# Kernel tuning notes

Hardware: AMD Instinct MI355X
Metric: run time of the kernel (lower is better)

Reference implementation:

```python
import jax, jax.numpy as jnp
import numpy as np

B, N, C, HEADS = 8, 1024, 768, 12
HW = 32  # H = W = 32, so H*W == N


def _layernorm(x, g, b, eps=1e-5):
    mu = x.mean(-1, keepdims=True)
    var = ((x - mu) ** 2).mean(-1, keepdims=True)
    return (x - mu) * jax.lax.rsqrt(var + eps) * g + b


def setup_inputs() -> dict:
    key = jax.random.key(0)
    ks = jax.random.split(key, 6)
    w = lambda k, shape: jax.random.normal(k, shape, dtype=jnp.float32) * 0.02
    return {
        "x": jax.random.normal(ks[0], (B, N, C), dtype=jnp.float32),
        "y": jax.random.normal(ks[1], (B, C, HW, HW), dtype=jnp.float32),
        "q_w": w(ks[2], (C, C)),
        "q_b": jnp.zeros((C,), jnp.float32),
        "kv_w": w(ks[3], (2 * C, C)),
        "kv_b": jnp.zeros((2 * C,), jnp.float32),
        "proj_w": w(ks[4], (C, C)),
        "proj_b": jnp.zeros((C,), jnp.float32),
        "ln_g": jnp.ones((C,), jnp.float32),
        "ln_b": jnp.zeros((C,), jnp.float32),
        "H": HW,
        "W": HW,
    }


def reference(x, y, q_w, q_b, kv_w, kv_b, proj_w, proj_b, ln_g, ln_b, H, W):
    Bn, Nn, Cn = x.shape
    hd = Cn // HEADS
    scale = hd ** -0.5  # qk_scale=None, c_ratio=1 -> head_dim**-0.5

    # gating tensors from y
    y1 = y.reshape(Bn, Cn, H * W).transpose(0, 2, 1)          # [B, N, C]
    y2 = _layernorm(y1, ln_g, ln_b)
    yq = jax.nn.sigmoid(y2 @ q_w.T + q_b)                      # [B, N, C]
    ykv = jax.nn.sigmoid(y2 @ kv_w.T + kv_b)                   # [B, N, 2C]

    # gated q: q2 = q0 + q0*yq
    q0 = x @ q_w.T + q_b
    q = (q0 + q0 * yq).reshape(Bn, Nn, HEADS, hd).transpose(0, 2, 1, 3)  # [B,h,N,d]

    # gated kv: kv2 = kv0*ykv + ykv
    kv0 = x @ kv_w.T + kv_b
    kv = (kv0 * ykv + ykv).reshape(Bn, Nn, 2, HEADS, hd).transpose(2, 0, 3, 1, 4)
    k, v = kv[0], kv[1]                                        # [B,h,N,d] each

    attn = jax.nn.softmax(jnp.einsum("bhqd,bhkd->bhqk", q, k) * scale, axis=-1)
    out = jnp.einsum("bhqk,bhkd->bhqd", attn, v)
    out = out.transpose(0, 2, 1, 3).reshape(Bn, Nn, Cn)
    return out @ proj_w.T + proj_b
```

## Files before the change

kernel.cpp:

```cpp
#include <hip/hip_runtime.h>
#include <stdint.h>

typedef __attribute__((ext_vector_type(4))) float f4;
typedef __attribute__((ext_vector_type(8))) short bf16x8;
typedef __attribute__((ext_vector_type(4))) unsigned short u16x4;
typedef unsigned short u16;

#define B_ 8
#define N_ 1024
#define C_ 768
#define NH 12
#define HD 64

__device__ __forceinline__ float bf2f(u16 v) {
  union { unsigned u; float f; } x; x.u = ((unsigned)v) << 16; return x.f;
}
__device__ __forceinline__ u16 f2bf(float f) {
  union { float f; unsigned u; } x; x.f = f;
  unsigned r = x.u + 0x7FFFu + ((x.u >> 16) & 1u);
  return (u16)(r >> 16);
}
__device__ __forceinline__ void g2l16(const u16* g, const u16* l) {
  __builtin_amdgcn_global_load_lds(
      (const __attribute__((address_space(1))) void*)(uintptr_t)g,
      (__attribute__((address_space(3))) void*)(uint32_t)(uintptr_t)l,
      16, 0, 0);
}

#define SW12() asm volatile("s_waitcnt vmcnt(12)" ::: "memory")
#define SW6()  asm volatile("s_waitcnt vmcnt(6)" ::: "memory")
#define SW4()  asm volatile("s_waitcnt vmcnt(4)" ::: "memory")
#define SW3()  asm volatile("s_waitcnt vmcnt(3)" ::: "memory")
#define SW0()  asm volatile("s_waitcnt vmcnt(0)" ::: "memory")
#define BARF()                              \
  do {                                      \
    __builtin_amdgcn_s_barrier();           \
    asm volatile("" ::: "memory");          \
    __builtin_amdgcn_sched_barrier(0);      \
  } while (0)

__global__ __launch_bounds__(256) void cvt_bf16(const float* __restrict__ s,
                                                u16* __restrict__ d, int n4) {
  int i = blockIdx.x * 256 + threadIdx.x;
  int stride = gridDim.x * 256;
  for (; i < n4; i += stride) {
    float4 v = ((const float4*)s)[i];
    u16x4 o;
    o.x = f2bf(v.x); o.y = f2bf(v.y); o.z = f2bf(v.z); o.w = f2bf(v.w);
    ((u16x4*)d)[i] = o;
  }
}

__global__ __launch_bounds__(256) void ln_stats(const float* __restrict__ y,
                                                float* __restrict__ mu,
                                                float* __restrict__ rs,
                                                int b0) {
  __shared__ float s1[4][64], s2[4][64];
  int t = threadIdx.x;
  int nl = t & 63, ch = t >> 6;
  int idx0 = b0 * N_ + blockIdx.x * 64;
  int b = idx0 >> 10, nb_ = idx0 & 1023;
  const float* p = y + (size_t)b * C_ * N_ + nb_ + nl;
  float s = 0.f, q = 0.f;
  int c0 = ch * 192;
  for (int c = c0; c < c0 + 192; ++c) {
    float v = p[(size_t)c * N_];
    s += v; q += v * v;
  }
  s1[ch][nl] = s; s2[ch][nl] = q;
  __syncthreads();
  if (t < 64) {
    float ts = s1[0][t] + s1[1][t] + s1[2][t] + s1[3][t];
    float tq = s2[0][t] + s2[1][t] + s2[2][t] + s2[3][t];
    float m = ts * (1.f / C_);
    float var = tq * (1.f / C_) - m * m;
    mu[idx0 + t] = m;
    rs[idx0 + t] = rsqrtf(fmaxf(var, 0.f) + 1e-5f);
  }
}

__global__ __launch_bounds__(256) void ln_apply(const float* __restrict__ y,
                                                const float* __restrict__ mu,
                                                const float* __restrict__ rs,
                                                const float* __restrict__ lg,
                                                const float* __restrict__ lb,
                                                u16* __restrict__ y2c,
                                                int b0) {
  __shared__ float tile[64][65];
  int t = threadIdx.x;
  int n0 = blockIdx.x * 64, c0 = blockIdx.y * 64;
  int bl = blockIdx.z, b = b0 + bl;
  int jc = (t & 15) * 4, ir = t >> 4;
  for (int r = 0; r < 4; ++r) {
    int i = ir + r * 16;
    float4 v = *(const float4*)(y + ((size_t)b * C_ + c0 + i) * N_ + n0 + jc);
    tile[i][jc] = v.x; tile[i][jc + 1] = v.y; tile[i][jc + 2] = v.z; tile[i][jc + 3] = v.w;
  }
  __syncthreads();
  for (int r = 0; r < 4; ++r) {
    int i = ir + r * 16;
    int n = n0 + i;
    float m = mu[b * N_ + n], rr = rs[b * N_ + n];
    float g0 = lg[c0 + jc],     b0f = lb[c0 + jc];
    float g1 = lg[c0 + jc + 1], b1f = lb[c0 + jc + 1];
    float g2 = lg[c0 + jc + 2], b2f = lb[c0 + jc + 2];
    float g3 = lg[c0 + jc + 3], b3f = lb[c0 + jc + 3];
    u16x4 o;
    o.x = f2bf((tile[jc][i] - m) * rr * g0 + b0f);
    o.y = f2bf((tile[jc + 1][i] - m) * rr * g1 + b1f);
    o.z = f2bf((tile[jc + 2][i] - m) * rr * g2 + b2f);
    o.w = f2bf((tile[jc + 3][i] - m) * rr * g3 + b3f);
    *(u16x4*)(y2c + ((size_t)bl * N_ + n) * C_ + c0 + jc) = o;
  }
}

__global__ __launch_bounds__(256, 2) void gemm_gate(
    const u16* __restrict__ xbc, const u16* __restrict__ y2c,
    const u16* __restrict__ qwb, const u16* __restrict__ kvwb,
    const float* __restrict__ qb_, const float* __restrict__ kvb_,
    u16* __restrict__ o_q, u16* __restrict__ o_k, u16* __restrict__ o_vT) {
  __shared__ u16 smem[36864];
  int t = threadIdx.x, l = t & 63;
  int quad = l >> 4, l15 = l & 15;
  int w = t >> 6, wm = w & 1, wn = w >> 1;
  int m0l = blockIdx.x * 128;
  int n0l = blockIdx.y * 128;

  const u16* wp; const float* bp; int sel, h0;
  if (n0l < C_) {
    wp = qwb + (size_t)n0l * C_; bp = qb_ + n0l; sel = 0; h0 = n0l >> 6;
  } else {
    int nk = n0l - C_;
    wp = kvwb + (size_t)nk * C_; bp = kvb_ + nk;
    sel = (nk < C_) ? 1 : 2;
    h0 = ((sel == 2) ? nk - C_ : nk) >> 6;
  }

  f4 accx[4][4], accy[4][4];
  for (int i = 0; i < 4; ++i)
    for (int j = 0; j < 4; ++j) {
      accx[i][j] = (f4){0.f, 0.f, 0.f, 0.f};
      accy[i][j] = (f4){0.f, 0.f, 0.f, 0.f};
    }

  int row = t >> 2;
  int colS = (((t & 3) ^ (row & 3)) * 8);
  const u16* gx = xbc + (size_t)(m0l + row) * C_ + colS;
  const u16* gy = y2c + (size_t)(m0l + row) * C_ + colS;
  const u16* gw = wp + (size_t)row * C_ + colS;
  int rsl = (quad ^ (l15 & 3)) * 8;

#define STAGE_G(OFF, kk)                                   \
  do {                                                     \
    u16* p_ = smem + (OFF);                                \
    g2l16(gx + (kk),           p_ + t * 8);                \
    g2l16(gx + (kk) + 64 * C_, p_ + 2048 + t * 8);         \
    g2l16(gy + (kk),           p_ + 4096 + t * 8);         \
    g2l16(gy + (kk) + 64 * C_, p_ + 6144 + t * 8);         \
    g2l16(gw + (kk),           p_ + 8192 + t * 8);         \
    g2l16(gw + (kk) + 64 * C_, p_ + 10240 + t * 8);        \
  } while (0)

#define COMPUTE_G(OFF)                                                        \
  do {                                                                        \
    const u16* base = smem + (OFF);                                           \
    bf16x8 afx[4], afy[4], bfr[4];                                            \
    for (int i = 0; i < 4; ++i) {                                             \
      int ra = (wm * 64 + i * 16 + l15) * 32 + rsl;                           \
      afx[i] = *(const bf16x8*)&base[ra];                                     \
      afy[i] = *(const bf16x8*)&base[4096 + ra];                              \
      int rb = (wn * 64 + i * 16 + l15) * 32 + rsl;                           \
      bfr[i] = *(const bf16x8*)&base[8192 + rb];                              \
    }                                                                         \
    for (int i = 0; i < 4; ++i)                                               \
      for (int j = 0; j < 4; ++j) {                                           \
        accx[i][j] = __builtin_amdgcn_mfma_f32_16x16x32_bf16(afx[i], bfr[j], accx[i][j], 0, 0, 0); \
        accy[i][j] = __builtin_amdgcn_mfma_f32_16x16x32_bf16(afy[i], bfr[j], accy[i][j], 0, 0, 0); \
      }                                                                       \
  } while (0)

#define STEP_G(i, OFF)                                        \
  do {                                                        \
    COMPUTE_G(OFF);                                           \
    BARF();                                                   \
    if ((i) < 21)      { STAGE_G(OFF, ((i) + 3) * 32); SW12(); } \
    else if ((i) == 21) SW6();                                \
    else if ((i) == 22) SW0();                                \
    BARF();                                                   \
  } while (0)

  STAGE_G(0, 0);
  STAGE_G(12288, 32);
  STAGE_G(24576, 64);
  SW12();
  BARF();
#pragma unroll
  for (int n = 0; n < 24; n += 3) {
    STEP_G(n, 0);
    STEP_G(n + 1, 12288);
    STEP_G(n + 2, 24576);
  }
#undef STEP_G
#undef STAGE_G
#undef COMPUTE_G

  const int PITCH = 136;
  for (int j = 0; j < 4; ++j) {
    int cloc = wn * 64 + j * 16 + l15;
    float bias = bp[cloc];
    for (int i = 0; i < 4; ++i) {
      int rb0 = wm * 64 + i * 16 + quad * 4;
      for (int r = 0; r < 4; ++r) {
        int rloc = rb0 + r;
        float vx = accx[i][j][r] + bias;
        float vy = accy[i][j][r] + bias;
        float gg = 1.f / (1.f + __expf(-vy));
        float val = (sel == 0) ? vx * (1.f + gg) : gg * (vx + 1.f);
        u16 bv = f2bf(val);
        if (sel == 2) smem[cloc * PITCH + rloc] = bv;
        else          smem[rloc * PITCH + cloc] = bv;
      }
    }
  }
  __syncthreads();
  {
    int rr = t >> 1, hh = t & 1;
    const u16* src = smem + rr * PITCH + hh * 64;
    u16* dst;
    if (sel == 2) {
      int h = h0 + (rr >> 6), d = rr & 63;
      int bl = m0l >> 10, nbase = m0l & 1023;
      dst = o_vT + (size_t)((bl * NH + h) * HD + d) * N_ + nbase + hh * 64;
    } else {
      int gml = m0l + rr;
      int bl = gml >> 10, n = gml & 1023;
      int h = h0 + hh;
      dst = (sel == 0 ? o_q : o_k) + (size_t)((bl * NH + h) * N_ + n) * HD;
    }
    for (int c = 0; c < 8; ++c) {
      bf16x8 v = *(const bf16x8*)(src + c * 8);
      *(bf16x8*)(dst + c * 8) = v;
    }
  }
}

__global__ __launch_bounds__(256) void attn(const u16* __restrict__ qoc,
                                            const u16* __restrict__ koc,
                                            const u16* __restrict__ vTc,
                                            u16* __restrict__ aoc) {
  __shared__ u16 Qs[4096], Ks[8192], Vs[8192];
  __shared__ u16 Ps[64 * 72];
  int t = threadIdx.x, l = t & 63, w = t >> 6;
  int quad = l >> 4, l15 = l & 15;
  int bhl = blockIdx.y;
  int bl = bhl / NH, h = bhl % NH;
  int q0 = blockIdx.x * 64;
  int sr = t >> 3;
  int swo = ((t & 7) ^ (sr & 7)) * 8;
  const u16* qbp = qoc + ((size_t)bhl * N_ + q0) * HD;
  const u16* kb = koc + (size_t)bhl * N_ * HD;
  const u16* vb = vTc + (size_t)bhl * HD * N_;

#define STAGE_KV(OFF, key0)                                                   \
  do {                                                                        \
    g2l16(kb + (size_t)((key0) + sr) * HD + swo,      Ks + (OFF) + t * 8);    \
    g2l16(kb + (size_t)((key0) + 32 + sr) * HD + swo, Ks + (OFF) + 2048 + t * 8); \
    g2l16(vb + (size_t)sr * N_ + (key0) + swo,        Vs + (OFF) + t * 8);    \
    g2l16(vb + (size_t)(32 + sr) * N_ + (key0) + swo, Vs + (OFF) + 2048 + t * 8); \
  } while (0)

  g2l16(qbp + sr * HD + swo,        Qs + t * 8);
  g2l16(qbp + (32 + sr) * HD + swo, Qs + 2048 + t * 8);
  STAGE_KV(0, 0);
  STAGE_KV(4096, 64);
  SW4();
  BARF();

  int sA = (quad ^ (l15 & 7)) * 8;
  int sB = sA ^ 32;
  bf16x8 aq0 = *(const bf16x8*)&Qs[(w * 16 + l15) * 64 + sA];
  bf16x8 aq1 = *(const bf16x8*)&Qs[(w * 16 + l15) * 64 + sB];
  f4 o[4];
  for (int i = 0; i < 4; ++i) o[i] = (f4){0.f, 0.f, 0.f, 0.f};
  f4 ls = (f4){0.f, 0.f, 0.f, 0.f};
  bf16x8 ones;
  for (int i = 0; i < 8; ++i) ones[i] = (short)0x3F80;

#define TILE_STEP(KOFF)                                                       \
  do {                                                                        \
    f4 s_[4];                                                                 \
    __builtin_amdgcn_s_setprio(1);                                            \
    for (int ni = 0; ni < 4; ++ni) {                                          \
      bf16x8 b0v = *(const bf16x8*)&Ks[(KOFF) + (ni * 16 + l15) * 64 + sA];   \
      bf16x8 b1v = *(const bf16x8*)&Ks[(KOFF) + (ni * 16 + l15) * 64 + sB];   \
      f4 z = (f4){0.f, 0.f, 0.f, 0.f};                                        \
      z = __builtin_amdgcn_mfma_f32_16x16x32_bf16(aq0, b0v, z, 0, 0, 0);      \
      z = __builtin_amdgcn_mfma_f32_16x16x32_bf16(aq1, b1v, z, 0, 0, 0);      \
      s_[ni] = z;                                                             \
    }                                                                         \
    __builtin_amdgcn_s_setprio(0);                                            \
    for (int ni = 0; ni < 4; ++ni)                                            \
      for (int r = 0; r < 4; ++r)                                             \
        Ps[(w * 16 + quad * 4 + r) * 72 + ni * 16 + l15] =                    \
            f2bf(__expf(s_[ni][r] * 0.125f));                                 \
    bf16x8 ap0 = *(const bf16x8*)&Ps[(w * 16 + l15) * 72 + quad * 8];         \
    bf16x8 ap1 = *(const bf16x8*)&Ps[(w * 16 + l15) * 72 + 32 + quad * 8];    \
    __builtin_amdgcn_s_setprio(1);                                            \
    for (int ni = 0; ni < 4; ++ni) {                                          \
      bf16x8 b0v = *(const bf16x8*)&Vs[(KOFF) + (ni * 16 + l15) * 64 + sA];   \
      bf16x8 b1v = *(const bf16x8*)&Vs[(KOFF) + (ni * 16 + l15) * 64 + sB];   \
      o[ni] = __builtin_amdgcn_mfma_f32_16x16x32_bf16(ap0, b0v, o[ni], 0, 0, 0); \
      o[ni] = __builtin_amdgcn_mfma_f32_16x16x32_bf16(ap1, b1v, o[ni], 0, 0, 0); \
    }                                                                         \
    ls = __builtin_amdgcn_mfma_f32_16x16x32_bf16(ap0, ones, ls, 0, 0, 0);     \
    ls = __builtin_amdgcn_mfma_f32_16x16x32_bf16(ap1, ones, ls, 0, 0, 0);     \
    __builtin_amdgcn_s_setprio(0);                                            \
  } while (0)

#pragma unroll
  for (int kt = 0; kt < 16; kt += 2) {
    TILE_STEP(0);
    BARF();
    if (kt + 2 < 16) { STAGE_KV(0, (kt + 2) * 64); SW4(); } else { SW0(); }
    BARF();
    TILE_STEP(4096);
    BARF();
    if (kt + 3 < 16) { STAGE_KV(4096, (kt + 3) * 64); SW4(); } else { SW0(); }
    BARF();
  }
#undef TILE_STEP
#undef STAGE_KV

  for (int ni = 0; ni < 4; ++ni)
    for (int r = 0; r < 4; ++r)
      Ps[(w * 16 + quad * 4 + r) * 72 + ni * 16 + l15] =
          f2bf(o[ni][r] / ls[r]);
  __syncthreads();
  {
    int rr = t >> 2, cc = t & 3;
    int n = q0 + rr;
    const u16* src = Ps + rr * 72 + cc * 16;
    u16* dst = aoc + ((size_t)bl * N_ + n) * C_ + h * HD + cc * 16;
    *(bf16x8*)dst = *(const bf16x8*)src;
    *(bf16x8*)(dst + 8) = *(const bf16x8*)(src + 8);
  }
}

__global__ __launch_bounds__(256, 2) void gemm_proj(const u16* __restrict__ aoc,
                                                    const u16* __restrict__ pwb,
                                                    const float* __restrict__ bias,
                                                    float* __restrict__ out,
                                                    int b0) {
  __shared__ u16 smem[18432];
  int t = threadIdx.x, l = t & 63;
  int quad = l >> 4, l15 = l & 15;
  int w = t >> 6, wm = w & 1, wn = w >> 1;
  int m0l = blockIdx.x * 128, n0 = blockIdx.y * 64;
  f4 acc[4][2];
  for (int i = 0; i < 4; ++i)
    for (int j = 0; j < 2; ++j) acc[i][j] = (f4){0.f, 0.f, 0.f, 0.f};
  int row = t >> 2;
  int colS = (((t & 3) ^ (row & 3)) * 8);
  const u16* ga = aoc + (size_t)(m0l + row) * C_ + colS;
  const u16* gw = pwb + (size_t)(n0 + row) * C_ + colS;
  int rsl = (quad ^ (l15 & 3)) * 8;

#define STAGE_P(OFF, kk)                                   \
  do {                                                     \
    u16* p_ = smem + (OFF);                                \
    g2l16(ga + (kk),           p_ + t * 8);                \
    g2l16(ga + (kk) + 64 * C_, p_ + 2048 + t * 8);         \
    g2l16(gw + (kk),           p_ + 4096 + t * 8);         \
  } while (0)

#define COMPUTE_P(OFF)                                                        \
  do {                                                                        \
    const u16* base = smem + (OFF);                                           \
    bf16x8 af[4], bfr[2];                                                     \
    for (int i = 0; i < 4; ++i)                                               \
      af[i] = *(const bf16x8*)&base[(wm * 64 + i * 16 + l15) * 32 + rsl];     \
    for (int j = 0; j < 2; ++j)                                               \
      bfr[j] = *(const bf16x8*)&base[4096 + (wn * 32 + j * 16 + l15) * 32 + rsl]; \
    for (int i = 0; i < 4; ++i)                                               \
      for (int j = 0; j < 2; ++j)                                             \
        acc[i][j] = __builtin_amdgcn_mfma_f32_16x16x32_bf16(af[i], bfr[j], acc[i][j], 0, 0, 0); \
  } while (0)

#define STEP_P(i, OFF)                                        \
  do {                                                        \
    COMPUTE_P(OFF);                                           \
    BARF();                                                   \
    if ((i) < 21)      { STAGE_P(OFF, ((i) + 3) * 32); SW6(); } \
    else if ((i) == 21) SW3();                                \
    else if ((i) == 22) SW0();                                \
    BARF();                                                   \
  } while (0)

  STAGE_P(0, 0);
  STAGE_P(6144, 32);
  STAGE_P(12288, 64);
  SW6();
  BARF();
#pragma unroll
  for (int n = 0; n < 24; n += 3) {
    STEP_P(n, 0);
    STEP_P(n + 1, 6144);
    STEP_P(n + 2, 12288);
  }
#undef STEP_P
#undef STAGE_P
#undef COMPUTE_P

  for (int j = 0; j < 2; ++j) {
    int gcol = n0 + wn * 32 + j * 16 + l15;
    float bv = bias[gcol];
    for (int i = 0; i < 4; ++i) {
      int rbase = m0l + wm * 64 + i * 16 + quad * 4;
      for (int r = 0; r < 4; ++r)
        __builtin_nontemporal_store(acc[i][j][r] + bv,
                                    &out[(size_t)(b0 * N_ + rbase + r) * C_ + gcol]);
    }
  }
}

extern "C" void kernel_launch(void* const* d_in, const int* in_sizes, int n_in,
                              void* d_out, int out_size, void* d_ws, size_t ws_size,
                              hipStream_t stream) {
  const float* x   = (const float*)d_in[0];
  const float* y   = (const float*)d_in[1];
  const float* qw  = (const float*)d_in[2];
  const float* qb  = (const float*)d_in[3];
  const float* kvw = (const float*)d_in[4];
  const float* kvb = (const float*)d_in[5];
  const float* pw  = (const float*)d_in[6];
  const float* pb  = (const float*)d_in[7];
  const float* lg  = (const float*)d_in[8];
  const float* lb  = (const float*)d_in[9];

  char* ws = (char*)d_ws;
  float* mu = (float*)(ws);
  float* rs = (float*)(ws + 32768);
  u16* qwb  = (u16*)(ws + 65536);
  u16* kvwb = (u16*)(ws + 1245184);
  u16* pwb  = (u16*)(ws + 3604480);
  const size_t BASE2 = 4784128;
  const size_t PER_B = 1572864;

  int nb = 1;
  for (int c = 8; c >= 1; c >>= 1) {
    if (BASE2 + 5 * (size_t)c * PER_B <= ws_size) { nb = c; break; }
  }
  u16* xbc = (u16*)(ws + BASE2);
  u16* y2c = (u16*)(ws + BASE2 + (size_t)nb * PER_B);
  u16* qoc = (u16*)(ws + BASE2 + 2 * (size_t)nb * PER_B);
  u16* koc = (u16*)(ws + BASE2 + 3 * (size_t)nb * PER_B);
  u16* vTc = (u16*)(ws + BASE2 + 4 * (size_t)nb * PER_B);
  u16* aoc = xbc;

  cvt_bf16<<<dim3(576), dim3(256), 0, stream>>>(qw, qwb, 147456);
  cvt_bf16<<<dim3(1152), dim3(256), 0, stream>>>(kvw, kvwb, 294912);
  cvt_bf16<<<dim3(576), dim3(256), 0, stream>>>(pw, pwb, 147456);

  for (int b0 = 0; b0 < B_; b0 += nb) {
    cvt_bf16<<<dim3(768 * nb), dim3(256), 0, stream>>>(
        x + (size_t)b0 * N_ * C_, xbc, nb * 196608);
    ln_stats<<<dim3(16 * nb), dim3(256), 0, stream>>>(y, mu, rs, b0);
    ln_apply<<<dim3(16, 12, nb), dim3(256), 0, stream>>>(y, mu, rs, lg, lb, y2c, b0);
    gemm_gate<<<dim3(8 * nb, 18), dim3(256), 0, stream>>>(xbc, y2c, qwb, kvwb,
                                                          qb, kvb, qoc, koc, vTc);
    attn<<<dim3(16, 12 * nb), dim3(256), 0, stream>>>(qoc, koc, vTc, aoc);
    gemm_proj<<<dim3(8 * nb, 12), dim3(256), 0, stream>>>(aoc, pwb, pb, (float*)d_out, b0);
  }
}
```

Before: 285.3 us.

## Issue next-stage global loads before compute with one barrier per K step

The gated-projection and output-projection GEMM loops now issue the async global-to-LDS stage for step i+2 into the free third buffer before computing on the current buffer, then wait once and barrier once per step instead of twice. This keeps prefetch distance at two and cuts one barrier per iteration while loads overlap the MFMA work. The pragma unroll directives on these loops and the attention loop are also removed, which may change code size and scheduling. The risk is reduced in-flight prefetch depth, and loops that are no longer fully unrolled may lose compile-time evaluation of the (i) conditions.

```diff
diff --git a/kernel.cpp b/kernel.cpp
--- a/kernel.cpp
+++ b/kernel.cpp
@@ -27,7 +27,6 @@
       16, 0, 0);
 }
 
-#define SW12() asm volatile("s_waitcnt vmcnt(12)" ::: "memory")
 #define SW6()  asm volatile("s_waitcnt vmcnt(6)" ::: "memory")
 #define SW4()  asm volatile("s_waitcnt vmcnt(4)" ::: "memory")
 #define SW3()  asm volatile("s_waitcnt vmcnt(3)" ::: "memory")
@@ -179,26 +178,23 @@
       }                                                                       \
   } while (0)
 
-#define STEP_G(i, OFF)                                        \
+#define STEP_G(i, OFFC, OFFS)                                 \
   do {                                                        \
-    COMPUTE_G(OFF);                                           \
-    BARF();                                                   \
-    if ((i) < 21)      { STAGE_G(OFF, ((i) + 3) * 32); SW12(); } \
-    else if ((i) == 21) SW6();                                \
+    if ((i) <= 21) STAGE_G(OFFS, ((i) + 2) * 32);             \
+    COMPUTE_G(OFFC);                                          \
+    if ((i) <= 21)      SW6();                                \
     else if ((i) == 22) SW0();                                \
     BARF();                                                   \
   } while (0)
 
   STAGE_G(0, 0);
   STAGE_G(12288, 32);
-  STAGE_G(24576, 64);
-  SW12();
+  SW6();
   BARF();
-#pragma unroll
   for (int n = 0; n < 24; n += 3) {
-    STEP_G(n, 0);
-    STEP_G(n + 1, 12288);
-    STEP_G(n + 2, 24576);
+    STEP_G(n,     0,     24576);
+    STEP_G(n + 1, 12288, 0);
+    STEP_G(n + 2, 24576, 12288);
   }
 #undef STEP_G
 #undef STAGE_G
@@ -317,7 +313,6 @@
     __builtin_amdgcn_s_setprio(0);                                            \
   } while (0)
 
-#pragma unroll
   for (int kt = 0; kt < 16; kt += 2) {
     TILE_STEP(0);
     BARF();
@@ -386,26 +381,23 @@
         acc[i][j] = __builtin_amdgcn_mfma_f32_16x16x32_bf16(af[i], bfr[j], acc[i][j], 0, 0, 0); \
   } while (0)
 
-#define STEP_P(i, OFF)                                        \
+#define STEP_P(i, OFFC, OFFS)                                 \
   do {                                                        \
-    COMPUTE_P(OFF);                                           \
-    BARF();                                                   \
-    if ((i) < 21)      { STAGE_P(OFF, ((i) + 3) * 32); SW6(); } \
-    else if ((i) == 21) SW3();                                \
+    if ((i) <= 21) STAGE_P(OFFS, ((i) + 2) * 32);             \
+    COMPUTE_P(OFFC);                                          \
+    if ((i) <= 21)      SW3();                                \
     else if ((i) == 22) SW0();                                \
     BARF();                                                   \
   } while (0)
 
   STAGE_P(0, 0);
   STAGE_P(6144, 32);
-  STAGE_P(12288, 64);
-  SW6();
+  SW3();
   BARF();
-#pragma unroll
   for (int n = 0; n < 24; n += 3) {
-    STEP_P(n, 0);
-    STEP_P(n + 1, 6144);
-    STEP_P(n + 2, 12288);
+    STEP_P(n,     0,     12288);
+    STEP_P(n + 1, 6144,  0);
+    STEP_P(n + 2, 12288, 6144);
   }
 #undef STEP_P
 #undef STAGE_P
```

Result: no change. 285.5 us (+0.1%).

## Double attention query tile to 128 rows and simplify proj GEMM pipeline

Applied to the files above, without the earlier changes.

The attention kernel now handles 128 query rows per block: each wave keeps two 16-row query fragments and reuses every staged K/V tile for both, so K/V global loads per query are halved. The grid shrinks to 8 blocks per head, which lowers parallelism and raises register and LDS use. The projection GEMM also drops from triple to double buffering and removes its LDS XOR swizzle, which may bring back bank conflicts in exchange for less shared memory.

```diff
diff --git a/kernel.cpp b/kernel.cpp
--- a/kernel.cpp
+++ b/kernel.cpp
@@ -248,13 +248,13 @@
                                             const u16* __restrict__ koc,
                                             const u16* __restrict__ vTc,
                                             u16* __restrict__ aoc) {
-  __shared__ u16 Qs[4096], Ks[8192], Vs[8192];
-  __shared__ u16 Ps[64 * 72];
+  __shared__ u16 Qs[8192], Ks[8192], Vs[8192];
+  __shared__ u16 Ps[128 * 72];
   int t = threadIdx.x, l = t & 63, w = t >> 6;
   int quad = l >> 4, l15 = l & 15;
   int bhl = blockIdx.y;
   int bl = bhl / NH, h = bhl % NH;
-  int q0 = blockIdx.x * 64;
+  int q0 = blockIdx.x * 128;
   int sr = t >> 3;
   int swo = ((t & 7) ^ (sr & 7)) * 8;
   const u16* qbp = qoc + ((size_t)bhl * N_ + q0) * HD;
@@ -269,8 +269,10 @@
     g2l16(vb + (size_t)(32 + sr) * N_ + (key0) + swo, Vs + (OFF) + 2048 + t * 8); \
   } while (0)
 
-  g2l16(qbp + sr * HD + swo,        Qs + t * 8);
-  g2l16(qbp + (32 + sr) * HD + swo, Qs + 2048 + t * 8);
+  g2l16(qbp + (size_t)(sr) * HD + swo,       Qs + t * 8);
+  g2l16(qbp + (size_t)(32 + sr) * HD + swo,  Qs + 2048 + t * 8);
+  g2l16(qbp + (size_t)(64 + sr) * HD + swo,  Qs + 4096 + t * 8);
+  g2l16(qbp + (size_t)(96 + sr) * HD + swo,  Qs + 6144 + t * 8);
   STAGE_KV(0, 0);
   STAGE_KV(4096, 64);
   SW4();
@@ -278,46 +280,68 @@
 
   int sA = (quad ^ (l15 & 7)) * 8;
   int sB = sA ^ 32;
-  bf16x8 aq0 = *(const bf16x8*)&Qs[(w * 16 + l15) * 64 + sA];
-  bf16x8 aq1 = *(const bf16x8*)&Qs[(w * 16 + l15) * 64 + sB];
-  f4 o[4];
-  for (int i = 0; i < 4; ++i) o[i] = (f4){0.f, 0.f, 0.f, 0.f};
-  f4 ls = (f4){0.f, 0.f, 0.f, 0.f};
+  bf16x8 aq00 = *(const bf16x8*)&Qs[(w * 16 + l15) * 64 + sA];
+  bf16x8 aq01 = *(const bf16x8*)&Qs[(w * 16 + l15) * 64 + sB];
+  bf16x8 aq10 = *(const bf16x8*)&Qs[(64 + w * 16 + l15) * 64 + sA];
+  bf16x8 aq11 = *(const bf16x8*)&Qs[(64 + w * 16 + l15) * 64 + sB];
+  f4 o0[4], o1[4];
+  for (int i = 0; i < 4; ++i) {
+    o0[i] = (f4){0.f, 0.f, 0.f, 0.f};
+    o1[i] = (f4){0.f, 0.f, 0.f, 0.f};
+  }
+  f4 ls0 = (f4){0.f, 0.f, 0.f, 0.f};
+  f4 ls1 = (f4){0.f, 0.f, 0.f, 0.f};
   bf16x8 ones;
   for (int i = 0; i < 8; ++i) ones[i] = (short)0x3F80;
 
 #define TILE_STEP(KOFF)                                                       \
   do {                                                                        \
-    f4 s_[4];                                                                 \
+    f4 s0_[4], s1_[4];                                                        \
     __builtin_amdgcn_s_setprio(1);                                            \
+    _Pragma("unroll")                                                         \
     for (int ni = 0; ni < 4; ++ni) {                                          \
       bf16x8 b0v = *(const bf16x8*)&Ks[(KOFF) + (ni * 16 + l15) * 64 + sA];   \
       bf16x8 b1v = *(const bf16x8*)&Ks[(KOFF) + (ni * 16 + l15) * 64 + sB];   \
-      f4 z = (f4){0.f, 0.f, 0.f, 0.f};                                        \
-      z = __builtin_amdgcn_mfma_f32_16x16x32_bf16(aq0, b0v, z, 0, 0, 0);      \
-      z = __builtin_amdgcn_mfma_f32_16x16x32_bf16(aq1, b1v, z, 0, 0, 0);      \
-      s_[ni] = z;                                                             \
+      f4 z0 = (f4){0.f, 0.f, 0.f, 0.f};                                       \
+      z0 = __builtin_amdgcn_mfma_f32_16x16x32_bf16(aq00, b0v, z0, 0, 0, 0);   \
+      z0 = __builtin_amdgcn_mfma_f32_16x16x32_bf16(aq01, b1v, z0, 0, 0, 0);   \
+      s0_[ni] = z0;                                                           \
+      f4 z1 = (f4){0.f, 0.f, 0.f, 0.f};                                       \
+      z1 = __builtin_amdgcn_mfma_f32_16x16x32_bf16(aq10, b0v, z1, 0, 0, 0);   \
+      z1 = __builtin_amdgcn_mfma_f32_16x16x32_bf16(aq11, b1v, z1, 0, 0, 0);   \
+      s1_[ni] = z1;                                                           \
     }                                                                         \
     __builtin_amdgcn_s_setprio(0);                                            \
+    _Pragma("unroll")                                                         \
     for (int ni = 0; ni < 4; ++ni)                                            \
-      for (int r = 0; r < 4; ++r)                                             \
+      _Pragma("unroll")                                                       \
+      for (int r = 0; r < 4; ++r) {                                           \
         Ps[(w * 16 + quad * 4 + r) * 72 + ni * 16 + l15] =                    \
-            f2bf(__expf(s_[ni][r] * 0.125f));                                 \
-    bf16x8 ap0 = *(const bf16x8*)&Ps[(w * 16 + l15) * 72 + quad * 8];         \
-    bf16x8 ap1 = *(const bf16x8*)&Ps[(w * 16 + l15) * 72 + 32 + quad * 8];    \
+            f2bf(__expf(s0_[ni][r] * 0.125f));                                \
+        Ps[(64 + w * 16 + quad * 4 + r) * 72 + ni * 16 + l15] =               \
+            f2bf(__expf(s1_[ni][r] * 0.125f));                                \
+      }                                                                       \
+    bf16x8 ap00 = *(const bf16x8*)&Ps[(w * 16 + l15) * 72 + quad * 8];        \
+    bf16x8 ap01 = *(const bf16x8*)&Ps[(w * 16 + l15) * 72 + 32 + quad * 8];   \
+    bf16x8 ap10 = *(const bf16x8*)&Ps[(64 + w * 16 + l15) * 72 + quad * 8];   \
+    bf16x8 ap11 = *(const bf16x8*)&Ps[(64 + w * 16 + l15) * 72 + 32 + quad * 8]; \
     __builtin_amdgcn_s_setprio(1);                                            \
+    _Pragma("unroll")                                                         \
     for (int ni = 0; ni < 4; ++ni) {                                          \
       bf16x8 b0v = *(const bf16x8*)&Vs[(KOFF) + (ni * 16 + l15) * 64 + sA];   \
       bf16x8 b1v = *(const bf16x8*)&Vs[(KOFF) + (ni * 16 + l15) * 64 + sB];   \
-      o[ni] = __builtin_amdgcn_mfma_f32_16x16x32_bf16(ap0, b0v, o[ni], 0, 0, 0); \
-      o[ni] = __builtin_amdgcn_mfma_f32_16x16x32_bf16(ap1, b1v, o[ni], 0, 0, 0); \
+      o0[ni] = __builtin_amdgcn_mfma_f32_16x16x32_bf16(ap00, b0v, o0[ni], 0, 0, 0); \
+      o0[ni] = __builtin_amdgcn_mfma_f32_16x16x32_bf16(ap01, b1v, o0[ni], 0, 0, 0); \
+      o1[ni] = __builtin_amdgcn_mfma_f32_16x16x32_bf16(ap10, b0v, o1[ni], 0, 0, 0); \
+      o1[ni] = __builtin_amdgcn_mfma_f32_16x16x32_bf16(ap11, b1v, o1[ni], 0, 0, 0); \
     }                                                                         \
-    ls = __builtin_amdgcn_mfma_f32_16x16x32_bf16(ap0, ones, ls, 0, 0, 0);     \
-    ls = __builtin_amdgcn_mfma_f32_16x16x32_bf16(ap1, ones, ls, 0, 0, 0);     \
+    ls0 = __builtin_amdgcn_mfma_f32_16x16x32_bf16(ap00, ones, ls0, 0, 0, 0);  \
+    ls0 = __builtin_amdgcn_mfma_f32_16x16x32_bf16(ap01, ones, ls0, 0, 0, 0);  \
+    ls1 = __builtin_amdgcn_mfma_f32_16x16x32_bf16(ap10, ones, ls1, 0, 0, 0);  \
+    ls1 = __builtin_amdgcn_mfma_f32_16x16x32_bf16(ap11, ones, ls1, 0, 0, 0);  \
     __builtin_amdgcn_s_setprio(0);                                            \
   } while (0)
 
-#pragma unroll
   for (int kt = 0; kt < 16; kt += 2) {
     TILE_STEP(0);
     BARF();
@@ -332,17 +356,20 @@
 #undef STAGE_KV
 
   for (int ni = 0; ni < 4; ++ni)
-    for (int r = 0; r < 4; ++r)
+    for (int r = 0; r < 4; ++r) {
       Ps[(w * 16 + quad * 4 + r) * 72 + ni * 16 + l15] =
-          f2bf(o[ni][r] / ls[r]);
+          f2bf(o0[ni][r] / ls0[r]);
+      Ps[(64 + w * 16 + quad * 4 + r) * 72 + ni * 16 + l15] =
+          f2bf(o1[ni][r] / ls1[r]);
+    }
   __syncthreads();
   {
-    int rr = t >> 2, cc = t & 3;
+    int rr = t >> 1, cc = t & 1;
     int n = q0 + rr;
-    const u16* src = Ps + rr * 72 + cc * 16;
-    u16* dst = aoc + ((size_t)bl * N_ + n) * C_ + h * HD + cc * 16;
-    *(bf16x8*)dst = *(const bf16x8*)src;
-    *(bf16x8*)(dst + 8) = *(const bf16x8*)(src + 8);
+    const u16* src = Ps + rr * 72 + cc * 32;
+    u16* dst = aoc + ((size_t)bl * N_ + n) * C_ + h * HD + cc * 32;
+    for (int c = 0; c < 4; ++c)
+      *(bf16x8*)(dst + c * 8) = *(const bf16x8*)(src + c * 8);
   }
 }
 
@@ -351,7 +378,7 @@
                                                     const float* __restrict__ bias,
                                                     float* __restrict__ out,
                                                     int b0) {
-  __shared__ u16 smem[18432];
+  __shared__ u16 smem[12288];
   int t = threadIdx.x, l = t & 63;
   int quad = l >> 4, l15 = l & 15;
   int w = t >> 6, wm = w & 1, wn = w >> 1;
@@ -359,11 +386,9 @@
   f4 acc[4][2];
   for (int i = 0; i < 4; ++i)
     for (int j = 0; j < 2; ++j) acc[i][j] = (f4){0.f, 0.f, 0.f, 0.f};
-  int row = t >> 2;
-  int colS = (((t & 3) ^ (row & 3)) * 8);
-  const u16* ga = aoc + (size_t)(m0l + row) * C_ + colS;
-  const u16* gw = pwb + (size_t)(n0 + row) * C_ + colS;
-  int rsl = (quad ^ (l15 & 3)) * 8;
+  int row = t >> 2, colb = (t & 3) * 8;
+  const u16* ga = aoc + (size_t)(m0l + row) * C_ + colb;
+  const u16* gw = pwb + (size_t)(n0 + row) * C_ + colb;
 
 #define STAGE_P(OFF, kk)                                   \
   do {                                                     \
@@ -378,36 +403,28 @@
     const u16* base = smem + (OFF);                                           \
     bf16x8 af[4], bfr[2];                                                     \
     for (int i = 0; i < 4; ++i)                                               \
-      af[i] = *(const bf16x8*)&base[(wm * 64 + i * 16 + l15) * 32 + rsl];     \
+      af[i] = *(const bf16x8*)&base[(wm * 64 + i * 16 + l15) * 32 + quad * 8];\
     for (int j = 0; j < 2; ++j)                                               \
-      bfr[j] = *(const bf16x8*)&base[4096 + (wn * 32 + j * 16 + l15) * 32 + rsl]; \
+      bfr[j] = *(const bf16x8*)&base[4096 + (wn * 32 + j * 16 + l15) * 32 + quad * 8]; \
     for (int i = 0; i < 4; ++i)                                               \
       for (int j = 0; j < 2; ++j)                                             \
         acc[i][j] = __builtin_amdgcn_mfma_f32_16x16x32_bf16(af[i], bfr[j], acc[i][j], 0, 0, 0); \
   } while (0)
 
-#define STEP_P(i, OFF)                                        \
-  do {                                                        \
-    COMPUTE_P(OFF);                                           \
-    BARF();                                                   \
-    if ((i) < 21)      { STAGE_P(OFF, ((i) + 3) * 32); SW6(); } \
-    else if ((i) == 21) SW3();                                \
-    else if ((i) == 22) SW0();                                \
-    BARF();                                                   \
-  } while (0)
-
   STAGE_P(0, 0);
   STAGE_P(6144, 32);
-  STAGE_P(12288, 64);
-  SW6();
+  SW3();
   BARF();
-#pragma unroll
-  for (int n = 0; n < 24; n += 3) {
-    STEP_P(n, 0);
-    STEP_P(n + 1, 6144);
-    STEP_P(n + 2, 12288);
-  }
-#undef STEP_P
+  for (int n = 0; n < 24; n += 2) {
+    COMPUTE_P(0);
+    BARF();
+    if (n + 2 < 24) { STAGE_P(0, (n + 2) * 32); SW3(); } else { SW0(); }
+    BARF();
+    COMPUTE_P(6144);
+    BARF();
+    if (n + 3 < 24) { STAGE_P(6144, (n + 3) * 32); SW3(); } else { SW0(); }
+    BARF();
+  }
 #undef STAGE_P
 #undef COMPUTE_P
 
@@ -468,7 +485,7 @@
     ln_apply<<<dim3(16, 12, nb), dim3(256), 0, stream>>>(y, mu, rs, lg, lb, y2c, b0);
     gemm_gate<<<dim3(8 * nb, 18), dim3(256), 0, stream>>>(xbc, y2c, qwb, kvwb,
                                                           qb, kvb, qoc, koc, vTc);
-    attn<<<dim3(16, 12 * nb), dim3(256), 0, stream>>>(qoc, koc, vTc, aoc);
+    attn<<<dim3(8, 12 * nb), dim3(256), 0, stream>>>(qoc, koc, vTc, aoc);
     gemm_proj<<<dim3(8 * nb, 12), dim3(256), 0, stream>>>(aoc, pwb, pb, (float*)d_out, b0);
   }
 }
```

New measurement: 284.7 us. Within noise of the previous version (-0.2%).
